# Performance work log

Measured on AMD Instinct MI355X. Metric: run time of the kernel, lower is better.

The kernel has to match this reference:

```python
import jax, jax.numpy as jnp
import numpy as np

B, NOTES, T, IN, H, NH = 32, 78, 128, 80, 128, 2  # batch, notes, time steps, input feats, time hidden, note hidden


def setup_inputs() -> dict:
    key = jax.random.key(0)
    ks = jax.random.split(key, 9)
    s = 0.1
    f32 = jnp.float32
    return {
        "x": jax.random.normal(ks[0], (B, NOTES, T, IN), f32),
        # time LSTM params (PyTorch layout: [4H, in], gate order i,f,g,o)
        "Wih_t": (jax.random.normal(ks[1], (4 * H, IN), f32) * s),
        "Whh_t": (jax.random.normal(ks[2], (4 * H, H), f32) * s),
        "bih_t": (jax.random.normal(ks[3], (4 * H,), f32) * s),
        "bhh_t": (jax.random.normal(ks[4], (4 * H,), f32) * s),
        # note LSTM params (hidden size 2)
        "Wih_n": (jax.random.normal(ks[5], (4 * NH, H), f32) * s),
        "Whh_n": (jax.random.normal(ks[6], (4 * NH, NH), f32) * s),
        "bih_n": (jax.random.normal(ks[7], (4 * NH,), f32) * s),
        "bhh_n": (jax.random.normal(ks[8], (4 * NH,), f32) * s),
    }


def _lstm(x, Wih, Whh, bih, bhh):
    # x: [N, L, in] -> all-step hidden states [N, L, H]; zero initial (h, c)
    N = x.shape[0]
    Hh = Whh.shape[1]
    b = bih + bhh

    def step(carry, xt):
        h, c = carry
        g = xt @ Wih.T + h @ Whh.T + b  # [N, 4H]
        i, f, gg, o = jnp.split(g, 4, axis=-1)
        c = jax.nn.sigmoid(f) * c + jax.nn.sigmoid(i) * jnp.tanh(gg)
        h = jax.nn.sigmoid(o) * jnp.tanh(c)
        return (h, c), h

    h0 = jnp.zeros((N, Hh), x.dtype)
    _, hs = jax.lax.scan(step, (h0, h0), x.transpose(1, 0, 2))  # hs: [L, N, H]
    return hs.transpose(1, 0, 2)


def reference(x, Wih_t, Whh_t, bih_t, bhh_t, Wih_n, Whh_n, bih_n, bhh_n):
    Bn = x.shape[0]
    # time LSTM: one sequence per (batch, note) -> batched into N = B*NOTES
    th = _lstm(x.reshape(Bn * NOTES, T, IN), Wih_t, Whh_t, bih_t, bhh_t)
    th = th.reshape(Bn, NOTES, T, H)
    # note LSTM: sequence over the 78-note axis at each time step -> batch B*T
    xn = th.transpose(0, 2, 1, 3).reshape(Bn * T, NOTES, H)
    nh = _lstm(xn, Wih_n, Whh_n, bih_n, bhh_n).reshape(Bn, T, NOTES, NH)
    return nh.reshape(Bn, T, NOTES * NH)  # [B, T, 156]
```

## Files before the change

### kernel.cpp

```cpp
#include <hip/hip_runtime.h>

#define B_     32
#define NOTES_ 78
#define T_     128
#define IN_    80
#define H_     128
#define NSEQ_  (B_*NOTES_)
#define MBLK   16
#define NBLK1  (NSEQ_/MBLK)
#define SEQ2_  (B_*T_)
#define XN8    (NSEQ_*T_*IN_/8)
#define SHSTR  136

typedef __attribute__((ext_vector_type(8))) short short8;
typedef __attribute__((ext_vector_type(4))) float f32x4;

__device__ __forceinline__ float bf2f(unsigned short v) {
    unsigned u = ((unsigned)v) << 16; float f; __builtin_memcpy(&f, &u, 4); return f;
}
__device__ __forceinline__ unsigned short f2bf(float f) {
    unsigned u; __builtin_memcpy(&u, &f, 4);
    u += 0x7fffu + ((u >> 16) & 1u);
    return (unsigned short)(u >> 16);
}
__device__ __forceinline__ short8 pack8(const float* p) {
    short8 r;
    #pragma unroll
    for (int k = 0; k < 8; ++k) r[k] = (short)f2bf(p[k]);
    return r;
}
__device__ __forceinline__ float rcpf(float x)  { return __builtin_amdgcn_rcpf(x); }
__device__ __forceinline__ float sigm(float x)  { return rcpf(1.f + __expf(-x)); }
__device__ __forceinline__ float tanh_(float x) { return 2.f * rcpf(1.f + __expf(-2.f*x)) - 1.f; }

__global__ __launch_bounds__(256) void xcvt_kernel(
    const float* __restrict__ x, unsigned short* __restrict__ xb)
{
    const int i = blockIdx.x * 256 + threadIdx.x;
    if (i < XN8) {
        const f32x4 a = *(const f32x4*)(x + (size_t)i * 8);
        const f32x4 b = *(const f32x4*)(x + (size_t)i * 8 + 4);
        short8 r;
        #pragma unroll
        for (int k = 0; k < 4; ++k) { r[k] = (short)f2bf(a[k]); r[4+k] = (short)f2bf(b[k]); }
        *(short8*)(xb + (size_t)i * 8) = r;
    }
}

template<bool XB16>
__global__ __launch_bounds__(512, 2) void time_lstm_kernel(
    const void* __restrict__ xin,
    const float* __restrict__ Wih,
    const float* __restrict__ Whh,
    const float* __restrict__ bih,
    const float* __restrict__ bhh,
    const float* __restrict__ Wn,
    const float* __restrict__ bn1,
    const float* __restrict__ bn2,
    float* __restrict__ Gn)
{
    __shared__ unsigned short sH[2][MBLK * SHSTR];

    const int tid  = threadIdx.x;
    const int wave = tid >> 6, lane = tid & 63;
    const int m16  = lane & 15, quad = lane >> 4;
    const int seq0 = blockIdx.x * MBLK;
    const int j    = wave * 16 + m16;

    for (int i = tid; i < 2 * MBLK * SHSTR; i += 512)
        ((unsigned short*)sH)[i] = 0;

    const short8 zero8 = (short8){0,0,0,0,0,0,0,0};
    short8 wf[4][3], hf[4][4];
    #pragma unroll
    for (int g = 0; g < 4; ++g) {
        const int n = g * H_ + j;
        #pragma unroll
        for (int kt = 0; kt < 3; ++kt) {
            const int k = kt * 32 + quad * 8;
            wf[g][kt] = (k < IN_) ? pack8(Wih + n * IN_ + k) : zero8;
        }
        #pragma unroll
        for (int kt = 0; kt < 4; ++kt)
            hf[g][kt] = pack8(Whh + n * H_ + kt * 32 + quad * 8);
    }

    short8 wn[4] = {zero8, zero8, zero8, zero8};
    float bns = 0.f;
    unsigned gbase[4] = {0, 0, 0, 0};
    if (wave == 0) {
        #pragma unroll
        for (int kt = 0; kt < 4; ++kt)
            wn[kt] = (m16 < 8) ? pack8(Wn + m16 * H_ + kt * 32 + quad * 8) : zero8;
        if (m16 < 8) bns = bn1[m16] + bn2[m16];
        #pragma unroll
        for (int r = 0; r < 4; ++r) {
            const int sq = seq0 + quad * 4 + r;
            const int bb = sq / NOTES_;
            const int nn = sq - bb * NOTES_;
            gbase[r] = ((unsigned)bb * (T_ * NOTES_) + (unsigned)nn) * 8u + (unsigned)m16;
        }
    }

    const float b_i = bih[      j] + bhh[      j];
    const float b_f = bih[128 + j] + bhh[128 + j];
    const float b_g = bih[256 + j] + bhh[256 + j];
    const float b_o = bih[384 + j] + bhh[384 + j];

    const float* xrf = XB16 ? nullptr
        : ((const float*)xin + (size_t)(seq0 + m16) * T_ * IN_);
    const unsigned short* xrb = XB16
        ? ((const unsigned short*)xin + (size_t)(seq0 + m16) * T_ * IN_) : nullptr;

    short8 ax0, ax1, ax2 = zero8;
    if (XB16) {
        const unsigned short* p = xrb;
        ax0 = *(const short8*)(p + quad * 8);
        ax1 = *(const short8*)(p + 32 + quad * 8);
        if (quad < 2) ax2 = *(const short8*)(p + 64 + quad * 8);
    } else {
        const float* p = xrf;
        ax0 = pack8(p + quad * 8);
        ax1 = pack8(p + 32 + quad * 8);
        if (quad < 2) ax2 = pack8(p + 64 + quad * 8);
    }

    float cst[4] = {0.f, 0.f, 0.f, 0.f};

    __syncthreads();

    for (int t = 0; t < T_; ++t) {
        const unsigned short* sHr = sH[t & 1];
        unsigned short*       sHw = sH[(t & 1) ^ 1];

        short8 ah[4];
        #pragma unroll
        for (int kt = 0; kt < 4; ++kt)
            ah[kt] = *(const short8*)(sHr + m16 * SHSTR + kt * 32 + quad * 8);

        if (wave == 0 && t > 0) {
            f32x4 an = (f32x4){0.f, 0.f, 0.f, 0.f};
            #pragma unroll
            for (int kt = 0; kt < 4; ++kt)
                an = __builtin_amdgcn_mfma_f32_16x16x32_bf16(ah[kt], wn[kt], an, 0, 0, 0);
            if (m16 < 8) {
                #pragma unroll
                for (int r = 0; r < 4; ++r)
                    Gn[gbase[r] + (unsigned)(t - 1) * (NOTES_ * 8)] = an[r] + bns;
            }
        }

        f32x4 acc[4];
        #pragma unroll
        for (int g = 0; g < 4; ++g) {
            acc[g] = (f32x4){0.f, 0.f, 0.f, 0.f};
            acc[g] = __builtin_amdgcn_mfma_f32_16x16x32_bf16(ax0, wf[g][0], acc[g], 0, 0, 0);
            acc[g] = __builtin_amdgcn_mfma_f32_16x16x32_bf16(ax1, wf[g][1], acc[g], 0, 0, 0);
            acc[g] = __builtin_amdgcn_mfma_f32_16x16x32_bf16(ax2, wf[g][2], acc[g], 0, 0, 0);
            #pragma unroll
            for (int kt = 0; kt < 4; ++kt)
                acc[g] = __builtin_amdgcn_mfma_f32_16x16x32_bf16(ah[kt], hf[g][kt], acc[g], 0, 0, 0);
        }

        if (t + 1 < T_) {
            if (XB16) {
                const unsigned short* p = xrb + (t + 1) * IN_;
                ax0 = *(const short8*)(p + quad * 8);
                ax1 = *(const short8*)(p + 32 + quad * 8);
                if (quad < 2) ax2 = *(const short8*)(p + 64 + quad * 8);
            } else {
                const float* p = xrf + (t + 1) * IN_;
                ax0 = pack8(p + quad * 8);
                ax1 = pack8(p + 32 + quad * 8);
                if (quad < 2) ax2 = pack8(p + 64 + quad * 8);
            }
        }

        #pragma unroll
        for (int r = 0; r < 4; ++r) {
            const float gi = acc[0][r] + b_i;
            const float gf = acc[1][r] + b_f;
            const float gg = acc[2][r] + b_g;
            const float go = acc[3][r] + b_o;
            const float cf = sigm(gf) * cst[r] + sigm(gi) * tanh_(gg);
            cst[r] = cf;
            const float h = sigm(go) * tanh_(cf);
            sHw[(quad * 4 + r) * SHSTR + j] = f2bf(h);
        }

        __builtin_amdgcn_sched_barrier(0);
        asm volatile("s_waitcnt lgkmcnt(0)" ::: "memory");
        __builtin_amdgcn_s_barrier();
        __builtin_amdgcn_sched_barrier(0);
    }

    if (wave == 0) {
        const unsigned short* sHr = sH[T_ & 1];
        short8 ah[4];
        #pragma unroll
        for (int kt = 0; kt < 4; ++kt)
            ah[kt] = *(const short8*)(sHr + m16 * SHSTR + kt * 32 + quad * 8);
        f32x4 an = (f32x4){0.f, 0.f, 0.f, 0.f};
        #pragma unroll
        for (int kt = 0; kt < 4; ++kt)
            an = __builtin_amdgcn_mfma_f32_16x16x32_bf16(ah[kt], wn[kt], an, 0, 0, 0);
        if (m16 < 8) {
            #pragma unroll
            for (int r = 0; r < 4; ++r)
                Gn[gbase[r] + (unsigned)(T_ - 1) * (NOTES_ * 8)] = an[r] + bns;
        }
    }
}

__global__ __launch_bounds__(64) void note_out_kernel(
    const float* __restrict__ Gn,
    const float* __restrict__ Whh,
    float* __restrict__ out)
{
    const int q = blockIdx.x * 64 + threadIdx.x;
    if (q >= SEQ2_) return;

    float w0[8], w1[8];
    #pragma unroll
    for (int g = 0; g < 8; ++g) { w0[g] = Whh[g * 2]; w1[g] = Whh[g * 2 + 1]; }

    const float* gp = Gn + (size_t)q * (NOTES_ * 8);
    float* op = out + (size_t)q * (NOTES_ * 2);

    float h0 = 0.f, h1 = 0.f, c0 = 0.f, c1 = 0.f;
    f32x4 ga = *(const f32x4*)(gp);
    f32x4 gb = *(const f32x4*)(gp + 4);
    for (int n = 0; n < NOTES_; ++n) {
        f32x4 na, nb;
        if (n + 1 < NOTES_) {
            na = *(const f32x4*)(gp + (n + 1) * 8);
            nb = *(const f32x4*)(gp + (n + 1) * 8 + 4);
        }
        const float i0 = ga[0] + w0[0] * h0 + w1[0] * h1;
        const float i1 = ga[1] + w0[1] * h0 + w1[1] * h1;
        const float f0 = ga[2] + w0[2] * h0 + w1[2] * h1;
        const float f1 = ga[3] + w0[3] * h0 + w1[3] * h1;
        const float g0 = gb[0] + w0[4] * h0 + w1[4] * h1;
        const float g1 = gb[1] + w0[5] * h0 + w1[5] * h1;
        const float o0 = gb[2] + w0[6] * h0 + w1[6] * h1;
        const float o1 = gb[3] + w0[7] * h0 + w1[7] * h1;
        c0 = sigm(f0) * c0 + sigm(i0) * tanh_(g0);
        c1 = sigm(f1) * c1 + sigm(i1) * tanh_(g1);
        h0 = sigm(o0) * tanh_(c0);
        h1 = sigm(o1) * tanh_(c1);
        op[n * 2 + 0] = h0;
        op[n * 2 + 1] = h1;
        ga = na; gb = nb;
    }
}

extern "C" void kernel_launch(void* const* d_in, const int* in_sizes, int n_in,
                              void* d_out, int out_size, void* d_ws, size_t ws_size,
                              hipStream_t stream) {
    const float* x     = (const float*)d_in[0];
    const float* Wih_t = (const float*)d_in[1];
    const float* Whh_t = (const float*)d_in[2];
    const float* bih_t = (const float*)d_in[3];
    const float* bhh_t = (const float*)d_in[4];
    const float* Wih_n = (const float*)d_in[5];
    const float* Whh_n = (const float*)d_in[6];
    const float* bih_n = (const float*)d_in[7];
    const float* bhh_n = (const float*)d_in[8];
    float* out = (float*)d_out;

    const size_t xb_bytes = (size_t)NSEQ_ * T_ * IN_ * 2;
    const size_t gn_bytes = (size_t)SEQ2_ * NOTES_ * 8 * 4;

    if (ws_size >= xb_bytes + gn_bytes) {
        unsigned short* xb = (unsigned short*)d_ws;
        float* Gn = (float*)((char*)d_ws + xb_bytes);
        xcvt_kernel<<<(XN8 + 255) / 256, 256, 0, stream>>>(x, xb);
        time_lstm_kernel<true><<<NBLK1, 512, 0, stream>>>(
            xb, Wih_t, Whh_t, bih_t, bhh_t, Wih_n, bih_n, bhh_n, Gn);
        note_out_kernel<<<SEQ2_ / 64, 64, 0, stream>>>(Gn, Whh_n, out);
    } else {
        float* Gn = (float*)d_ws;
        time_lstm_kernel<false><<<NBLK1, 512, 0, stream>>>(
            x, Wih_t, Whh_t, bih_t, bhh_t, Wih_n, bih_n, bhh_n, Gn);
        note_out_kernel<<<SEQ2_ / 64, 64, 0, stream>>>(Gn, Whh_n, out);
    }
}
```

Before: 437.0 us.

## Software-pipeline input projection one step ahead and rotate note-projection across waves

Computes the input-to-gate MFMAs for step t+1 (with bias folded into the accumulator init) after the recurrent MFMAs of step t, so they sit off the serial h-dependency chain. Input loads are prefetched two steps ahead. The note-LSTM input projection and Gn store rotate among the 8 waves instead of always running on wave 0, spreading that extra work. This costs more registers (accX plus all waves holding wn and gbase), which may reduce occupancy.

```diff
diff --git a/kernel.cpp b/kernel.cpp
--- a/kernel.cpp
+++ b/kernel.cpp
@@ -85,27 +85,23 @@
             hf[g][kt] = pack8(Whh + n * H_ + kt * 32 + quad * 8);
     }
 
-    short8 wn[4] = {zero8, zero8, zero8, zero8};
-    float bns = 0.f;
-    unsigned gbase[4] = {0, 0, 0, 0};
-    if (wave == 0) {
-        #pragma unroll
-        for (int kt = 0; kt < 4; ++kt)
-            wn[kt] = (m16 < 8) ? pack8(Wn + m16 * H_ + kt * 32 + quad * 8) : zero8;
-        if (m16 < 8) bns = bn1[m16] + bn2[m16];
-        #pragma unroll
-        for (int r = 0; r < 4; ++r) {
-            const int sq = seq0 + quad * 4 + r;
-            const int bb = sq / NOTES_;
-            const int nn = sq - bb * NOTES_;
-            gbase[r] = ((unsigned)bb * (T_ * NOTES_) + (unsigned)nn) * 8u + (unsigned)m16;
-        }
-    }
-
-    const float b_i = bih[      j] + bhh[      j];
-    const float b_f = bih[128 + j] + bhh[128 + j];
-    const float b_g = bih[256 + j] + bhh[256 + j];
-    const float b_o = bih[384 + j] + bhh[384 + j];
+    short8 wn[4];
+    #pragma unroll
+    for (int kt = 0; kt < 4; ++kt)
+        wn[kt] = (m16 < 8) ? pack8(Wn + m16 * H_ + kt * 32 + quad * 8) : zero8;
+    const float bns = (m16 < 8) ? (bn1[m16] + bn2[m16]) : 0.f;
+    unsigned gbase[4];
+    #pragma unroll
+    for (int r = 0; r < 4; ++r) {
+        const int sq = seq0 + quad * 4 + r;
+        const int bb = sq / NOTES_;
+        const int nn = sq - bb * NOTES_;
+        gbase[r] = ((unsigned)bb * (T_ * NOTES_) + (unsigned)nn) * 8u + (unsigned)m16;
+    }
+
+    float bg4[4];
+    #pragma unroll
+    for (int g = 0; g < 4; ++g) bg4[g] = bih[g * H_ + j] + bhh[g * H_ + j];
 
     const float* xrf = XB16 ? nullptr
         : ((const float*)xin + (size_t)(seq0 + m16) * T_ * IN_);
@@ -125,6 +121,26 @@
         if (quad < 2) ax2 = pack8(p + 64 + quad * 8);
     }
 
+    f32x4 accX[4];
+    #pragma unroll
+    for (int g = 0; g < 4; ++g) {
+        accX[g] = (f32x4){bg4[g], bg4[g], bg4[g], bg4[g]};
+        accX[g] = __builtin_amdgcn_mfma_f32_16x16x32_bf16(ax0, wf[g][0], accX[g], 0, 0, 0);
+        accX[g] = __builtin_amdgcn_mfma_f32_16x16x32_bf16(ax1, wf[g][1], accX[g], 0, 0, 0);
+        accX[g] = __builtin_amdgcn_mfma_f32_16x16x32_bf16(ax2, wf[g][2], accX[g], 0, 0, 0);
+    }
+    if (XB16) {
+        const unsigned short* p = xrb + IN_;
+        ax0 = *(const short8*)(p + quad * 8);
+        ax1 = *(const short8*)(p + 32 + quad * 8);
+        if (quad < 2) ax2 = *(const short8*)(p + 64 + quad * 8);
+    } else {
+        const float* p = xrf + IN_;
+        ax0 = pack8(p + quad * 8);
+        ax1 = pack8(p + 32 + quad * 8);
+        if (quad < 2) ax2 = pack8(p + 64 + quad * 8);
+    }
+
     float cst[4] = {0.f, 0.f, 0.f, 0.f};
 
     __syncthreads();
@@ -138,7 +154,16 @@
         for (int kt = 0; kt < 4; ++kt)
             ah[kt] = *(const short8*)(sHr + m16 * SHSTR + kt * 32 + quad * 8);
 
-        if (wave == 0 && t > 0) {
+        f32x4 acc[4];
+        #pragma unroll
+        for (int g = 0; g < 4; ++g) {
+            acc[g] = accX[g];
+            #pragma unroll
+            for (int kt = 0; kt < 4; ++kt)
+                acc[g] = __builtin_amdgcn_mfma_f32_16x16x32_bf16(ah[kt], hf[g][kt], acc[g], 0, 0, 0);
+        }
+
+        if (t > 0 && wave == ((t - 1) & 7)) {
             f32x4 an = (f32x4){0.f, 0.f, 0.f, 0.f};
             #pragma unroll
             for (int kt = 0; kt < 4; ++kt)
@@ -150,26 +175,24 @@
             }
         }
 
-        f32x4 acc[4];
-        #pragma unroll
-        for (int g = 0; g < 4; ++g) {
-            acc[g] = (f32x4){0.f, 0.f, 0.f, 0.f};
-            acc[g] = __builtin_amdgcn_mfma_f32_16x16x32_bf16(ax0, wf[g][0], acc[g], 0, 0, 0);
-            acc[g] = __builtin_amdgcn_mfma_f32_16x16x32_bf16(ax1, wf[g][1], acc[g], 0, 0, 0);
-            acc[g] = __builtin_amdgcn_mfma_f32_16x16x32_bf16(ax2, wf[g][2], acc[g], 0, 0, 0);
+        if (t + 1 < T_) {
             #pragma unroll
-            for (int kt = 0; kt < 4; ++kt)
-                acc[g] = __builtin_amdgcn_mfma_f32_16x16x32_bf16(ah[kt], hf[g][kt], acc[g], 0, 0, 0);
-        }
-
-        if (t + 1 < T_) {
+            for (int g = 0; g < 4; ++g) {
+                accX[g] = (f32x4){bg4[g], bg4[g], bg4[g], bg4[g]};
+                accX[g] = __builtin_amdgcn_mfma_f32_16x16x32_bf16(ax0, wf[g][0], accX[g], 0, 0, 0);
+                accX[g] = __builtin_amdgcn_mfma_f32_16x16x32_bf16(ax1, wf[g][1], accX[g], 0, 0, 0);
+                accX[g] = __builtin_amdgcn_mfma_f32_16x16x32_bf16(ax2, wf[g][2], accX[g], 0, 0, 0);
+            }
+        }
+
+        if (t + 2 < T_) {
             if (XB16) {
-                const unsigned short* p = xrb + (t + 1) * IN_;
+                const unsigned short* p = xrb + (t + 2) * IN_;
                 ax0 = *(const short8*)(p + quad * 8);
                 ax1 = *(const short8*)(p + 32 + quad * 8);
                 if (quad < 2) ax2 = *(const short8*)(p + 64 + quad * 8);
             } else {
-                const float* p = xrf + (t + 1) * IN_;
+                const float* p = xrf + (t + 2) * IN_;
                 ax0 = pack8(p + quad * 8);
                 ax1 = pack8(p + 32 + quad * 8);
                 if (quad < 2) ax2 = pack8(p + 64 + quad * 8);
@@ -178,13 +201,9 @@
 
         #pragma unroll
         for (int r = 0; r < 4; ++r) {
-            const float gi = acc[0][r] + b_i;
-            const float gf = acc[1][r] + b_f;
-            const float gg = acc[2][r] + b_g;
-            const float go = acc[3][r] + b_o;
-            const float cf = sigm(gf) * cst[r] + sigm(gi) * tanh_(gg);
+            const float cf = sigm(acc[1][r]) * cst[r] + sigm(acc[0][r]) * tanh_(acc[2][r]);
             cst[r] = cf;
-            const float h = sigm(go) * tanh_(cf);
+            const float h = sigm(acc[3][r]) * tanh_(cf);
             sHw[(quad * 4 + r) * SHSTR + j] = f2bf(h);
         }
 
@@ -194,7 +213,7 @@
         __builtin_amdgcn_sched_barrier(0);
     }
 
-    if (wave == 0) {
+    if (wave == ((T_ - 1) & 7)) {
         const unsigned short* sHr = sH[T_ & 1];
         short8 ah[4];
         #pragma unroll
```

Measured after the change: 375.9 us. -14.0%, faster.
